# Performance work log

Hardware: AMD Instinct MI355X
Metric: run time of the kernel (lower is better)

Reference implementation:

```python
import jax, jax.numpy as jnp
import numpy as np

NUM_HEADS = 8
KEY_DIM = 32
ATTN_RATIO = 4
RESOLUTION = 7
VAL_DIM = KEY_DIM * ATTN_RATIO  # 128
SCALE = KEY_DIM ** (-0.5)


def _bias_idxs():
    # (2, N) grid positions, N = resolution^2
    r = RESOLUTION
    gh, gw = np.meshgrid(np.arange(r), np.arange(r), indexing='ij')
    pos = np.stack([gh, gw], 0).reshape(2, -1)
    rel = np.abs(pos[:, :, None] - pos[:, None, :])
    return jnp.asarray(rel[0] * r + rel[1], dtype=jnp.int32)  # (N, N)


def setup_inputs() -> dict:
    key = jax.random.key(0)
    ks = jax.random.split(key, 4)
    B, N, D = 2048, RESOLUTION * RESOLUTION, 384
    qkv_out = KEY_DIM * NUM_HEADS * 2 + VAL_DIM * NUM_HEADS  # 1536
    return {
        'x': jax.random.normal(ks[0], (B, N, D), jnp.float32),
        'qkv_kernel': jax.random.normal(ks[1], (D, qkv_out), jnp.float32) * 0.02,
        'qkv_bias': jnp.zeros((qkv_out,), jnp.float32),
        'proj_kernel': jax.random.normal(ks[2], (VAL_DIM * NUM_HEADS, D), jnp.float32) * 0.02,
        'proj_bias': jnp.zeros((D,), jnp.float32),
        'attention_biases': jax.random.normal(ks[3], (NUM_HEADS, N), jnp.float32) * 0.02,
    }


def reference(x, qkv_kernel, qkv_bias, proj_kernel, proj_bias, attention_biases):
    B, N, _ = x.shape
    idxs = _bias_idxs()  # (N, N) int32
    qkv = jnp.matmul(x, qkv_kernel) + qkv_bias            # (B, N, 1536)
    qkv = qkv.reshape(B, N, NUM_HEADS, -1).transpose(0, 2, 1, 3)  # (B, H, N, 2k+v)
    q = qkv[..., :KEY_DIM]
    k = qkv[..., KEY_DIM:2 * KEY_DIM]
    v = qkv[..., 2 * KEY_DIM:]
    attn = jnp.einsum('bhnd,bhmd->bhnm', q, k) * SCALE    # (B, H, N, N)
    bias = attention_biases[:, idxs]                       # (H, N, N) gather
    attn = jax.nn.softmax(attn + bias, axis=-1)
    out = jnp.einsum('bhnm,bhmd->bhnd', attn, v)           # (B, H, N, val_dim)
    out = out.transpose(0, 2, 1, 3).reshape(B, N, NUM_HEADS * VAL_DIM)
    return jnp.matmul(out, proj_kernel) + proj_bias
```

## Files before the change

### kernel.cpp

```cpp
#include <hip/hip_runtime.h>
#include <hip/hip_bf16.h>

using bf16x8 = short __attribute__((ext_vector_type(8)));
using f32x16 = float __attribute__((ext_vector_type(16)));

#define MROWS 100352
#define SCALE_Q 0.17677669529663687f

static __device__ __forceinline__ unsigned short f2bs(float f){
  unsigned u = __builtin_bit_cast(unsigned, f);
  unsigned r = (u + 0x7FFFu + ((u >> 16) & 1u)) >> 16;
  return (unsigned short)r;
}
static __device__ __forceinline__ unsigned packbf(float a, float b){
  return (unsigned)f2bs(a) | ((unsigned)f2bs(b) << 16);
}

__global__ void k_convert(const float* __restrict__ qkvW, const float* __restrict__ qkvB,
                          const float* __restrict__ projW, const float* __restrict__ ab,
                          short* __restrict__ WqkvT, short* __restrict__ WpT,
                          float* __restrict__ bqkv, float* __restrict__ bias_exp){
  int i = blockIdx.x*256 + threadIdx.x;
  if (i < 1536*384){
    int c = i/384, f = i - c*384;
    int src; float sc = 1.0f;
    if (c < 512){ src = (c>>6)*192 + (c&63); if ((c&63) < 32) sc = SCALE_Q; }
    else        { int dv = c - 512; src = (dv>>7)*192 + 64 + (dv&127); }
    WqkvT[i] = (short)f2bs(qkvW[f*1536 + src] * sc);
    return;
  }
  i -= 1536*384;
  if (i < 384*1024){
    int j = i/1024, m = i - j*1024;
    WpT[i] = (short)f2bs(projW[m*384 + j]);
    return;
  }
  i -= 384*1024;
  if (i < 1536){
    int c = i; int src; float sc = 1.0f;
    if (c < 512){ src = (c>>6)*192 + (c&63); if ((c&63) < 32) sc = SCALE_Q; }
    else        { int dv = c - 512; src = (dv>>7)*192 + 64 + (dv&127); }
    bqkv[c] = qkvB[src] * sc;
    return;
  }
  i -= 1536;
  if (i < 8*64*49){
    int h = i / (64*49), rem = i - h*(64*49);
    int r = rem / 49, n = rem - r*49;
    float v = 0.0f;
    if (r < 49){
      int rh = r/7, rw = r - rh*7, ch = n/7, cw = n - ch*7;
      int dh = rh>ch?rh-ch:ch-rh, dw = rw>cw?rw-cw:cw-rw;
      v = ab[h*49 + dh*7 + dw];
    }
    bias_exp[i] = v;
  }
}

__global__ __launch_bounds__(256) void k_qkv4(const float* __restrict__ x,
                                              const short* __restrict__ WqkvT,
                                              const float* __restrict__ bqkv,
                                              short* __restrict__ qkvbuf){
  __shared__ short Alds[128*64];
  __shared__ short Blds[2][256*64];
  const int t = threadIdx.x;
  const int lane = t & 63, w = t >> 6;
  const int hi = lane >> 5, l31 = lane & 31;
  const int wm = w >> 1, wn = w & 1;

  const int nwg = 6*784;
  const int lin = blockIdx.x + 6*blockIdx.y;
  const int swz = (lin & 7)*(nwg>>3) + (lin>>3);
  const int slab = swz % 6, panel = swz / 6;
  const size_t R0 = (size_t)panel*128, C0 = (size_t)slab*256;

  const int rs = t >> 1, hb = t & 1;
  const float* xrow = x + (R0 + rs)*384 + hb*32;
  const int srow = lane >> 3;
  const int sG = ((lane & 7) ^ srow) * 8;
  const short* bG = WqkvT + (C0 + (size_t)(w*8 + srow))*384 + sG;

  float4 ar[8];

  #pragma unroll
  for (int i=0; i<8; ++i) ar[i] = *reinterpret_cast<const float4*>(xrow + i*4);
  #pragma unroll
  for (int i=0; i<4; ++i){
    const float4 u0 = ar[2*i], u1 = ar[2*i+1];
    bf16x8 tt;
    tt[0]=(short)f2bs(u0.x); tt[1]=(short)f2bs(u0.y); tt[2]=(short)f2bs(u0.z); tt[3]=(short)f2bs(u0.w);
    tt[4]=(short)f2bs(u1.x); tt[5]=(short)f2bs(u1.y); tt[6]=(short)f2bs(u1.z); tt[7]=(short)f2bs(u1.w);
    const int clog = hb*4 + i;
    *reinterpret_cast<bf16x8*>(&Alds[rs*64 + ((clog ^ (rs&7))<<3)]) = tt;
  }
  #pragma unroll
  for (int j=0; j<8; ++j)
    __builtin_amdgcn_global_load_lds(
      (const unsigned int __attribute__((address_space(1)))*)(bG + (size_t)j*32*384),
      (unsigned int __attribute__((address_space(3)))*)(&Blds[0][(j*32 + w*8)*64]), 16, 0, 0);
  __syncthreads();

  f32x16 acc[2][4];
  #pragma unroll
  for (int mt=0; mt<2; ++mt)
    #pragma unroll
    for (int nt=0; nt<4; ++nt) acc[mt][nt] = (f32x16)0.0f;

  for (int kt=0; kt<6; ++kt){
    const int cur = kt & 1;
    if (kt < 5){
      #pragma unroll
      for (int j=0; j<8; ++j)
        __builtin_amdgcn_global_load_lds(
          (const unsigned int __attribute__((address_space(1)))*)(bG + (size_t)j*32*384 + (kt+1)*64),
          (unsigned int __attribute__((address_space(3)))*)(&Blds[cur^1][(j*32 + w*8)*64]), 16, 0, 0);
      #pragma unroll
      for (int i=0; i<8; ++i)
        ar[i] = *reinterpret_cast<const float4*>(xrow + (kt+1)*64 + i*4);
    }
    #pragma unroll
    for (int ks=0; ks<4; ++ks){
      bf16x8 aF[2], bF[4];
      #pragma unroll
      for (int mt=0; mt<2; ++mt){
        const int rA = wm*64 + mt*32 + l31;
        aF[mt] = *reinterpret_cast<const bf16x8*>(
                   (const char*)Alds + rA*128 + ((((ks<<1)|hi) ^ (rA&7))<<4));
      }
      #pragma unroll
      for (int nt=0; nt<4; ++nt){
        const int rB = wn*128 + nt*32 + l31;
        bF[nt] = *reinterpret_cast<const bf16x8*>(
                   (const char*)Blds[cur] + rB*128 + ((((ks<<1)|hi) ^ (rB&7))<<4));
      }
      #pragma unroll
      for (int mt=0; mt<2; ++mt)
        #pragma unroll
        for (int nt=0; nt<4; ++nt)
          acc[mt][nt] = __builtin_amdgcn_mfma_f32_32x32x16_bf16(aF[mt], bF[nt], acc[mt][nt], 0,0,0);
    }
    if (kt < 5){
      __syncthreads();
      #pragma unroll
      for (int i=0; i<4; ++i){
        const float4 u0 = ar[2*i], u1 = ar[2*i+1];
        bf16x8 tt;
        tt[0]=(short)f2bs(u0.x); tt[1]=(short)f2bs(u0.y); tt[2]=(short)f2bs(u0.z); tt[3]=(short)f2bs(u0.w);
        tt[4]=(short)f2bs(u1.x); tt[5]=(short)f2bs(u1.y); tt[6]=(short)f2bs(u1.z); tt[7]=(short)f2bs(u1.w);
        const int clog = hb*4 + i;
        *reinterpret_cast<bf16x8*>(&Alds[rs*64 + ((clog ^ (rs&7))<<3)]) = tt;
      }
      __syncthreads();
    }
  }

  #pragma unroll
  for (int nt=0; nt<4; ++nt){
    const int c = (int)C0 + wn*128 + nt*32 + l31;
    const float bb = bqkv[c];
    #pragma unroll
    for (int mt=0; mt<2; ++mt){
      const size_t rbase = R0 + wm*64 + mt*32;
      #pragma unroll
      for (int rg=0; rg<16; ++rg){
        const size_t r = rbase + (rg&3) + 8*(rg>>2) + 4*hi;
        qkvbuf[r*1536 + c] = (short)f2bs(acc[mt][nt][rg] + bb);
      }
    }
  }
}

__global__ __launch_bounds__(256) void k_proj4(const short* __restrict__ A,
                                               const short* __restrict__ Bw,
                                               const float* __restrict__ bias,
                                               float* __restrict__ out){
  __shared__ short Alds[128*64];
  __shared__ short Blds[128*64];
  const int lane = threadIdx.x & 63, w = threadIdx.x >> 6;
  const int hi = lane >> 5, l31 = lane & 31;
  const int wm = w >> 1, wn = w & 1;

  const int nwg = 3 * 784;
  const int lin = blockIdx.x + 3 * blockIdx.y;
  const int swz = (lin & 7) * (nwg >> 3) + (lin >> 3);
  const int slab = swz % 3, panel = swz / 3;
  const size_t R0 = (size_t)panel * 128, C0 = (size_t)slab * 128;

  f32x16 acc[2][2];
  acc[0][0]=(f32x16)0.f; acc[0][1]=(f32x16)0.f; acc[1][0]=(f32x16)0.f; acc[1][1]=(f32x16)0.f;

  const int srow = lane >> 3;
  const int sG   = ((lane & 7) ^ srow) * 8;
  const short* aG = A  + (R0 + (size_t)(w*8 + srow))*1024 + sG;
  const short* bG = Bw + (C0 + (size_t)(w*8 + srow))*1024 + sG;

  for (int kt=0; kt<16; ++kt){
    #pragma unroll
    for (int j=0; j<4; ++j){
      __builtin_amdgcn_global_load_lds(
        (const unsigned int __attribute__((address_space(1)))*)(aG + (size_t)j*32*1024 + kt*64),
        (unsigned int __attribute__((address_space(3)))*)(&Alds[(j*32 + w*8)*64]), 16, 0, 0);
      __builtin_amdgcn_global_load_lds(
        (const unsigned int __attribute__((address_space(1)))*)(bG + (size_t)j*32*1024 + kt*64),
        (unsigned int __attribute__((address_space(3)))*)(&Blds[(j*32 + w*8)*64]), 16, 0, 0);
    }
    __syncthreads();
    #pragma unroll
    for (int ks=0; ks<4; ++ks){
      bf16x8 aF[2], bF[2];
      #pragma unroll
      for (int mt=0; mt<2; ++mt){
        const int rA = wm*64 + mt*32 + l31;
        aF[mt] = *reinterpret_cast<const bf16x8*>(
                   (const char*)Alds + rA*128 + ((((ks<<1)|hi) ^ (rA&7))<<4));
      }
      #pragma unroll
      for (int nt=0; nt<2; ++nt){
        const int rB = wn*64 + nt*32 + l31;
        bF[nt] = *reinterpret_cast<const bf16x8*>(
                   (const char*)Blds + rB*128 + ((((ks<<1)|hi) ^ (rB&7))<<4));
      }
      #pragma unroll
      for (int mt=0; mt<2; ++mt)
        #pragma unroll
        for (int nt=0; nt<2; ++nt)
          acc[mt][nt] = __builtin_amdgcn_mfma_f32_32x32x16_bf16(aF[mt], bF[nt], acc[mt][nt], 0,0,0);
    }
    __syncthreads();
  }

  #pragma unroll
  for (int nt=0; nt<2; ++nt){
    const int c = (int)C0 + wn*64 + nt*32 + l31;
    const float bb = bias[c];
    #pragma unroll
    for (int mt=0; mt<2; ++mt){
      const size_t rbase = R0 + wm*64 + mt*32;
      #pragma unroll
      for (int rg=0; rg<16; ++rg){
        const size_t r = rbase + (rg&3) + 8*(rg>>2) + 4*hi;
        out[r*384 + c] = acc[mt][nt][rg] + bb;
      }
    }
  }
}

__global__ __launch_bounds__(256) void k_attn(const short* __restrict__ qkvbuf,
                                              const float* __restrict__ bias_exp, short* __restrict__ aout){
  const int lane = threadIdx.x & 63, w = threadIdx.x >> 6;
  const int hi = lane >> 5, l31 = lane & 31;
  const int b = blockIdx.x, hg = blockIdx.y;
  const int h = hg*4 + w;

  __shared__ short vlds[4*49*136];

  for (int i=0; i<13; ++i){
    const int n = i*4 + w;
    if (n < 49){
      const bf16x8 vv = *reinterpret_cast<const bf16x8*>(qkvbuf + (b*49+n)*1536 + 512 + hg*512 + lane*8);
      const int hh = lane >> 4;
      const int d0 = ((lane & 15) * 8) ^ (((n>>3)&1) << 5);
      *reinterpret_cast<bf16x8*>(&vlds[(hh*49 + n)*136 + d0]) = vv;
    }
  }
  __syncthreads();

  bf16x8 kf[2][2];
  #pragma unroll
  for (int mt=0; mt<2; ++mt){
    const int n = 32*mt + l31;
    #pragma unroll
    for (int ks=0; ks<2; ++ks)
      kf[mt][ks] = (n < 49)
        ? *reinterpret_cast<const bf16x8*>(qkvbuf + (b*49+n)*1536 + h*64 + 32 + ks*16 + hi*8)
        : (bf16x8)(short)0;
  }
  const short* vb = &vlds[w*49*136];
  const int dxbase = hi << 5;

  for (int rb=0; rb<2; ++rb){
    const int r = 32*rb + l31;
    bf16x8 qf[2];
    #pragma unroll
    for (int ks=0; ks<2; ++ks)
      qf[ks] = (r < 49)
        ? *reinterpret_cast<const bf16x8*>(qkvbuf + (b*49+r)*1536 + h*64 + ks*16 + hi*8)
        : (bf16x8)(short)0;

    f32x16 s[2];
    s[0] = (f32x16)0.0f; s[1] = (f32x16)0.0f;
    #pragma unroll
    for (int ks=0; ks<2; ++ks){
      s[0] = __builtin_amdgcn_mfma_f32_32x32x16_bf16(kf[0][ks], qf[ks], s[0], 0, 0, 0);
      s[1] = __builtin_amdgcn_mfma_f32_32x32x16_bf16(kf[1][ks], qf[ks], s[1], 0, 0, 0);
    }

    float mloc = -3.0e38f;
    #pragma unroll
    for (int mt=0; mt<2; ++mt)
      #pragma unroll
      for (int rg=0; rg<16; ++rg){
        const int n = 32*mt + (rg&3) + 8*(rg>>2) + 4*hi;
        float v = s[mt][rg];
        v = (n < 49) ? v + bias_exp[(h*64 + r)*49 + n] : -1.0e30f;
        s[mt][rg] = v;
        mloc = fmaxf(mloc, v);
      }
    const float mrow = fmaxf(mloc, __shfl_xor(mloc, 32));
    float sloc = 0.0f;
    #pragma unroll
    for (int mt=0; mt<2; ++mt)
      #pragma unroll
      for (int rg=0; rg<16; ++rg){
        const float p = __expf(s[mt][rg] - mrow);
        s[mt][rg] = p; sloc += p;
      }
    const float inv = 1.0f / (sloc + __shfl_xor(sloc, 32));
    #pragma unroll
    for (int mt=0; mt<2; ++mt)
      #pragma unroll
      for (int rg=0; rg<16; ++rg) s[mt][rg] *= inv;

    unsigned pk[8][2];
    #pragma unroll
    for (int o=0; o<8; ++o){
      const int mt = o>>2, base = 4*(o&3);
      pk[o][0] = packbf(s[mt][base+0], s[mt][base+1]);
      pk[o][1] = packbf(s[mt][base+2], s[mt][base+3]);
    }
    bf16x8 af[4];
    #pragma unroll
    for (int ks=0; ks<4; ++ks){
      const unsigned e0 = pk[2*ks][0],   e1 = pk[2*ks][1];
      const unsigned o0 = pk[2*ks+1][0], o1 = pk[2*ks+1][1];
      const unsigned own0 = hi ? o0 : e0, own1 = hi ? o1 : e1;
      const unsigned oth0 = hi ? e0 : o0, oth1 = hi ? e1 : o1;
      const unsigned sw0 = __shfl_xor(oth0, 32), sw1 = __shfl_xor(oth1, 32);
      const unsigned lo0 = hi ? sw0 : own0, lo1 = hi ? sw1 : own1;
      const unsigned h0  = hi ? own0 : sw0, h1  = hi ? own1 : sw1;
      union { bf16x8 v; unsigned u[4]; } t;
      t.u[0]=lo0; t.u[1]=lo1; t.u[2]=h0; t.u[3]=h1;
      af[ks] = t.v;
    }

    #pragma unroll
    for (int dt=0; dt<4; ++dt){
      const int dx = (dt*32 + l31) ^ dxbase;
      f32x16 acc = (f32x16)0.0f;
      #pragma unroll
      for (int ks=0; ks<4; ++ks){
        bf16x8 t;
        if (ks < 3){
          const int nb = ks*16 + hi*8;
          #pragma unroll
          for (int j=0; j<8; ++j) t[j] = vb[(nb + j)*136 + dx];
        } else {
          #pragma unroll
          for (int j=0; j<8; ++j) t[j] = 0;
          if (hi == 0) t[0] = vb[48*136 + (dt*32 + l31)];
        }
        acc = __builtin_amdgcn_mfma_f32_32x32x16_bf16(af[ks], t, acc, 0, 0, 0);
      }
      #pragma unroll
      for (int rg=0; rg<16; ++rg){
        const int rr = 32*rb + (rg&3) + 8*(rg>>2) + 4*hi;
        if (rr < 49)
          aout[(b*49+rr)*1024 + h*128 + dt*32 + l31] = (short)f2bs(acc[rg]);
      }
    }
  }
}

extern "C" void kernel_launch(void* const* d_in, const int* in_sizes, int n_in,
                              void* d_out, int out_size, void* d_ws, size_t ws_size,
                              hipStream_t stream) {
  const float* x     = (const float*)d_in[0];
  const float* qkvW  = (const float*)d_in[1];
  const float* qkvB  = (const float*)d_in[2];
  const float* projW = (const float*)d_in[3];
  const float* projB = (const float*)d_in[4];
  const float* ab    = (const float*)d_in[5];

  char* ws = (char*)d_ws;
  short* aoutb = (short*)ws;
  size_t off = (size_t)MROWS*1024*2;
  short* qkvbuf = (short*)(ws + off); off += (size_t)MROWS*1536*2;
  short* WqkvT  = (short*)(ws + off); off += (size_t)1536*384*2;
  short* WpT    = (short*)(ws + off); off += (size_t)384*1024*2;
  float* bqkv   = (float*)(ws + off); off += (size_t)1536*4;
  float* bias_exp = (float*)(ws + off); off += (size_t)8*64*49*4;
  if (ws_size < off) return;

  const int conv_total = 1536*384 + 384*1024 + 1536 + 8*64*49;
  k_convert<<<(conv_total + 255)/256, 256, 0, stream>>>(qkvW, qkvB, projW, ab,
                                                        WqkvT, WpT, bqkv, bias_exp);
  k_qkv4<<<dim3(6, 784), 256, 0, stream>>>(x, WqkvT, bqkv, qkvbuf);
  k_attn<<<dim3(2048, 2), 256, 0, stream>>>(qkvbuf, bias_exp, aoutb);
  k_proj4<<<dim3(3, 784), 256, 0, stream>>>(aoutb, WpT, projB, (float*)d_out);
}
```

Measured before the change: 521.1 us.

## Pre-cast x to bf16 and use 256x256 QKV GEMM tiles with async LDS loads

A new kernel converts x from fp32 to bf16 once, into workspace that aliases the later attention-output buffer. The QKV GEMM then loads both A and B tiles straight into LDS with global_load_lds, dropping the in-loop register conversion. It also grows to 512 threads and 256x256 output tiles so each loaded tile feeds more MFMA work. In exchange it adds a full extra pass over x to write the bf16 copy. It also drops the double-buffered B prefetch, so loads no longer overlap compute within a block.

Measured after the change: 507.9 us. -2.5%, faster.

```diff
diff --git a/kernel.cpp b/kernel.cpp
--- a/kernel.cpp
+++ b/kernel.cpp
@@ -14,6 +14,16 @@
 }
 static __device__ __forceinline__ unsigned packbf(float a, float b){
   return (unsigned)f2bs(a) | ((unsigned)f2bs(b) << 16);
+}
+
+__global__ void k_xcast(const float* __restrict__ x, short* __restrict__ xb){
+  const int i = blockIdx.x*256 + threadIdx.x;
+  const float4 u0 = *reinterpret_cast<const float4*>(x + (size_t)i*8);
+  const float4 u1 = *reinterpret_cast<const float4*>(x + (size_t)i*8 + 4);
+  bf16x8 t;
+  t[0]=(short)f2bs(u0.x); t[1]=(short)f2bs(u0.y); t[2]=(short)f2bs(u0.z); t[3]=(short)f2bs(u0.w);
+  t[4]=(short)f2bs(u1.x); t[5]=(short)f2bs(u1.y); t[6]=(short)f2bs(u1.z); t[7]=(short)f2bs(u1.w);
+  *reinterpret_cast<bf16x8*>(xb + (size_t)i*8) = t;
 }
 
 __global__ void k_convert(const float* __restrict__ qkvW, const float* __restrict__ qkvB,
@@ -57,47 +67,36 @@
   }
 }
 
-__global__ __launch_bounds__(256) void k_qkv4(const float* __restrict__ x,
+__global__ __launch_bounds__(512) void k_qkv5(const short* __restrict__ xb,
                                               const short* __restrict__ WqkvT,
                                               const float* __restrict__ bqkv,
                                               short* __restrict__ qkvbuf){
-  __shared__ short Alds[128*64];
-  __shared__ short Blds[2][256*64];
-  const int t = threadIdx.x;
-  const int lane = t & 63, w = t >> 6;
+  __shared__ short Alds[256*64];
+  __shared__ short Blds[256*64];
+  const int lane = threadIdx.x & 63, w = threadIdx.x >> 6;
   const int hi = lane >> 5, l31 = lane & 31;
   const int wm = w >> 1, wn = w & 1;
 
-  const int nwg = 6*784;
+  const int nwg = 6*392;
   const int lin = blockIdx.x + 6*blockIdx.y;
   const int swz = (lin & 7)*(nwg>>3) + (lin>>3);
   const int slab = swz % 6, panel = swz / 6;
-  const size_t R0 = (size_t)panel*128, C0 = (size_t)slab*256;
-
-  const int rs = t >> 1, hb = t & 1;
-  const float* xrow = x + (R0 + rs)*384 + hb*32;
+  const size_t R0 = (size_t)panel*256, C0 = (size_t)slab*256;
+
   const int srow = lane >> 3;
-  const int sG = ((lane & 7) ^ srow) * 8;
+  const int sG   = ((lane & 7) ^ srow) * 8;
+  const short* aG = xb    + (R0 + (size_t)(w*8 + srow))*384 + sG;
   const short* bG = WqkvT + (C0 + (size_t)(w*8 + srow))*384 + sG;
 
-  float4 ar[8];
-
-  #pragma unroll
-  for (int i=0; i<8; ++i) ar[i] = *reinterpret_cast<const float4*>(xrow + i*4);
-  #pragma unroll
-  for (int i=0; i<4; ++i){
-    const float4 u0 = ar[2*i], u1 = ar[2*i+1];
-    bf16x8 tt;
-    tt[0]=(short)f2bs(u0.x); tt[1]=(short)f2bs(u0.y); tt[2]=(short)f2bs(u0.z); tt[3]=(short)f2bs(u0.w);
-    tt[4]=(short)f2bs(u1.x); tt[5]=(short)f2bs(u1.y); tt[6]=(short)f2bs(u1.z); tt[7]=(short)f2bs(u1.w);
-    const int clog = hb*4 + i;
-    *reinterpret_cast<bf16x8*>(&Alds[rs*64 + ((clog ^ (rs&7))<<3)]) = tt;
-  }
-  #pragma unroll
-  for (int j=0; j<8; ++j)
+  #pragma unroll
+  for (int j=0; j<4; ++j){
     __builtin_amdgcn_global_load_lds(
-      (const unsigned int __attribute__((address_space(1)))*)(bG + (size_t)j*32*384),
-      (unsigned int __attribute__((address_space(3)))*)(&Blds[0][(j*32 + w*8)*64]), 16, 0, 0);
+      (const unsigned int __attribute__((address_space(1)))*)(aG + (size_t)j*64*384),
+      (unsigned int __attribute__((address_space(3)))*)(&Alds[(j*64 + w*8)*64]), 16, 0, 0);
+    __builtin_amdgcn_global_load_lds(
+      (const unsigned int __attribute__((address_space(1)))*)(bG + (size_t)j*64*384),
+      (unsigned int __attribute__((address_space(3)))*)(&Blds[(j*64 + w*8)*64]), 16, 0, 0);
+  }
   __syncthreads();
 
   f32x16 acc[2][4];
@@ -107,17 +106,6 @@
     for (int nt=0; nt<4; ++nt) acc[mt][nt] = (f32x16)0.0f;
 
   for (int kt=0; kt<6; ++kt){
-    const int cur = kt & 1;
-    if (kt < 5){
-      #pragma unroll
-      for (int j=0; j<8; ++j)
-        __builtin_amdgcn_global_load_lds(
-          (const unsigned int __attribute__((address_space(1)))*)(bG + (size_t)j*32*384 + (kt+1)*64),
-          (unsigned int __attribute__((address_space(3)))*)(&Blds[cur^1][(j*32 + w*8)*64]), 16, 0, 0);
-      #pragma unroll
-      for (int i=0; i<8; ++i)
-        ar[i] = *reinterpret_cast<const float4*>(xrow + (kt+1)*64 + i*4);
-    }
     #pragma unroll
     for (int ks=0; ks<4; ++ks){
       bf16x8 aF[2], bF[4];
@@ -131,7 +119,7 @@
       for (int nt=0; nt<4; ++nt){
         const int rB = wn*128 + nt*32 + l31;
         bF[nt] = *reinterpret_cast<const bf16x8*>(
-                   (const char*)Blds[cur] + rB*128 + ((((ks<<1)|hi) ^ (rB&7))<<4));
+                   (const char*)Blds + rB*128 + ((((ks<<1)|hi) ^ (rB&7))<<4));
       }
       #pragma unroll
       for (int mt=0; mt<2; ++mt)
@@ -139,16 +127,16 @@
         for (int nt=0; nt<4; ++nt)
           acc[mt][nt] = __builtin_amdgcn_mfma_f32_32x32x16_bf16(aF[mt], bF[nt], acc[mt][nt], 0,0,0);
     }
+    __syncthreads();
     if (kt < 5){
-      __syncthreads();
-      #pragma unroll
-      for (int i=0; i<4; ++i){
-        const float4 u0 = ar[2*i], u1 = ar[2*i+1];
-        bf16x8 tt;
-        tt[0]=(short)f2bs(u0.x); tt[1]=(short)f2bs(u0.y); tt[2]=(short)f2bs(u0.z); tt[3]=(short)f2bs(u0.w);
-        tt[4]=(short)f2bs(u1.x); tt[5]=(short)f2bs(u1.y); tt[6]=(short)f2bs(u1.z); tt[7]=(short)f2bs(u1.w);
-        const int clog = hb*4 + i;
-        *reinterpret_cast<bf16x8*>(&Alds[rs*64 + ((clog ^ (rs&7))<<3)]) = tt;
+      #pragma unroll
+      for (int j=0; j<4; ++j){
+        __builtin_amdgcn_global_load_lds(
+          (const unsigned int __attribute__((address_space(1)))*)(aG + (size_t)j*64*384 + (kt+1)*64),
+          (unsigned int __attribute__((address_space(3)))*)(&Alds[(j*64 + w*8)*64]), 16, 0, 0);
+        __builtin_amdgcn_global_load_lds(
+          (const unsigned int __attribute__((address_space(1)))*)(bG + (size_t)j*64*384 + (kt+1)*64),
+          (unsigned int __attribute__((address_space(3)))*)(&Blds[(j*64 + w*8)*64]), 16, 0, 0);
       }
       __syncthreads();
     }
@@ -383,6 +371,7 @@
 
   char* ws = (char*)d_ws;
   short* aoutb = (short*)ws;
+  short* xb    = (short*)ws;
   size_t off = (size_t)MROWS*1024*2;
   short* qkvbuf = (short*)(ws + off); off += (size_t)MROWS*1536*2;
   short* WqkvT  = (short*)(ws + off); off += (size_t)1536*384*2;
@@ -394,7 +383,8 @@
   const int conv_total = 1536*384 + 384*1024 + 1536 + 8*64*49;
   k_convert<<<(conv_total + 255)/256, 256, 0, stream>>>(qkvW, qkvB, projW, ab,
                                                         WqkvT, WpT, bqkv, bias_exp);
-  k_qkv4<<<dim3(6, 784), 256, 0, stream>>>(x, WqkvT, bqkv, qkvbuf);
+  k_xcast<<<MROWS*384/8/256, 256, 0, stream>>>(x, xb);
+  k_qkv5<<<dim3(6, 392), 512, 0, stream>>>(xb, WqkvT, bqkv, qkvbuf);
   k_attn<<<dim3(2048, 2), 256, 0, stream>>>(qkvbuf, bias_exp, aoutb);
   k_proj4<<<dim3(3, 784), 256, 0, stream>>>(aoutb, WpT, projB, (float*)d_out);
 }
```
